# Kernel tuning notes

Hardware: AMD Instinct MI355X
Metric: run time of the kernel (lower is better)

Reference implementation:

```python
import jax, jax.numpy as jnp
import numpy as np

THRESHOLD = 6.0  # bnb MatmulLtState outlier threshold


def setup_inputs() -> dict:
    key = jax.random.key(0)
    k1, k2, k3, k4, k5 = jax.random.split(key, 5)
    B, S, DIN, DOUT = 4, 2048, 4096, 16384
    x = jax.random.normal(k1, (B, S, DIN), dtype=jnp.float32).astype(jnp.float16)
    # inject a few outlier feature columns (|x| > threshold) so the LLM.int8()
    # mixed-precision decomposition path is actually exercised
    out_cols = jax.random.randint(k5, (8,), 0, DIN)
    x = x.at[:, :, out_cols].multiply(10.0)
    # CB: int8 codebook values stored as fp16 (bnb keeps them as int8; math is identical)
    CB = jnp.round(jax.random.uniform(k2, (DOUT, DIN), minval=-127.0, maxval=127.0)).astype(jnp.float16)
    SCB = jax.random.uniform(k3, (DOUT, 1), minval=0.5, maxval=2.0).astype(jnp.float16)
    bias = (jax.random.normal(k4, (DOUT,)) * 0.01).astype(jnp.float16)
    return {"x": x, "CB": CB, "SCB": SCB, "bias": bias}


def _llm_int8_matmul(x, CB, SCB, bias, threshold):
    # forward: weight = CB * SCB / 127 (dequantized fp16 weight), then bnb's
    # mixed int8 matmul with outlier-column decomposition (has_fp16_weights=True)
    W = CB.astype(jnp.float32) * SCB.astype(jnp.float32) / 127.0  # [DOUT, DIN]
    xf = x.astype(jnp.float32)
    lead = xf.shape[:-1]
    X = xf.reshape(-1, xf.shape[-1])  # [N, DIN]

    # outlier columns: any row has |x| > threshold in that feature column
    col_out = (jnp.abs(X) > threshold).any(axis=0)  # [DIN] bool
    X_out = jnp.where(col_out[None, :], X, 0.0)      # fp16-path activations
    X_in = jnp.where(col_out[None, :], 0.0, X)       # int8-path activations

    # per-row (per-token) absmax int8 quantization of inlier activations
    sx = jnp.maximum(jnp.max(jnp.abs(X_in), axis=1, keepdims=True), 1e-8)  # [N,1]
    Xq = jnp.clip(jnp.round(X_in * (127.0 / sx)), -127.0, 127.0)

    # per-output-row absmax int8 quantization of the (dequantized) weight
    sw = jnp.maximum(jnp.max(jnp.abs(W), axis=1, keepdims=True), 1e-8)  # [DOUT,1]
    Wq = jnp.clip(jnp.round(W * (127.0 / sw)), -127.0, 127.0)

    # int8 GEMM (emulated in fp32) + dequant with outer product of scales
    out = (Xq @ Wq.T) * (sx * sw.T) * (1.0 / (127.0 * 127.0))  # [N, DOUT]
    # fp16 outlier path: only the outlier weight columns participate
    out = out + X_out @ jnp.where(col_out[None, :], W, 0.0).T
    out = out + bias.astype(jnp.float32)[None, :]
    return out.reshape(*lead, W.shape[0]).astype(jnp.float16)


def reference(x, CB, SCB, bias):
    return _llm_int8_matmul(x, CB, SCB, bias, THRESHOLD)
```

## Files before the change

### kernel.cpp

```cpp
#include <hip/hip_runtime.h>
#include <hip/hip_fp16.h>
#include <stdint.h>

typedef int v4i __attribute__((ext_vector_type(4)));

__device__ __forceinline__ void gld_lds16(const void* g, void* l) {
    __builtin_amdgcn_global_load_lds(
        (const __attribute__((address_space(1))) void*)g,
        (__attribute__((address_space(3))) void*)l,
        16, 0, 0);
}

#define ENDBAR() do { __builtin_amdgcn_s_barrier(); __builtin_amdgcn_sched_barrier(0); } while (0)
#define VMC(n)   asm volatile("s_waitcnt vmcnt(" #n ")" ::: "memory")
#define VMLG0()  asm volatile("s_waitcnt vmcnt(0) lgkmcnt(0)" ::: "memory")

__global__ __launch_bounds__(256) void k_flags(const float* __restrict__ x,
                                               unsigned int* __restrict__ flags,
                                               int total4, int DIN) {
    int idx = blockIdx.x * blockDim.x + threadIdx.x;
    int stride = gridDim.x * blockDim.x;
    int dmask = DIN - 1;
    for (int i = idx; i < total4; i += stride) {
        float4 v = ((const float4*)x)[i];
        int base = i * 4;
        if (fabsf(v.x) > 6.0f) atomicOr(&flags[(base + 0) & dmask], 1u);
        if (fabsf(v.y) > 6.0f) atomicOr(&flags[(base + 1) & dmask], 1u);
        if (fabsf(v.z) > 6.0f) atomicOr(&flags[(base + 2) & dmask], 1u);
        if (fabsf(v.w) > 6.0f) atomicOr(&flags[(base + 3) & dmask], 1u);
    }
}

__global__ __launch_bounds__(256) void k_build(const unsigned int* __restrict__ flags,
                                               unsigned char* __restrict__ bmask,
                                               int* __restrict__ ncols,
                                               int* __restrict__ cols, int DIN) {
    __shared__ int wcnt[4];
    __shared__ int base;
    int tid = threadIdx.x, lane = tid & 63, wid = tid >> 6;
    if (tid == 0) base = 0;
    __syncthreads();
    for (int c0 = 0; c0 < DIN; c0 += 256) {
        int c = c0 + tid;
        bool p = (c < DIN) && (flags[c] != 0u);
        if (c < DIN) bmask[c] = p ? 1 : 0;
        unsigned long long m = __ballot(p);
        int wpre = __popcll(m & ((1ull << lane) - 1ull));
        if (lane == 0) wcnt[wid] = __popcll(m);
        __syncthreads();
        int pre = 0;
        for (int w = 0; w < wid; w++) pre += wcnt[w];
        if (p) cols[base + pre + wpre] = c;
        __syncthreads();
        if (tid == 0) base += wcnt[0] + wcnt[1] + wcnt[2] + wcnt[3];
        __syncthreads();
    }
    if (tid == 0) *ncols = base;
}

__global__ __launch_bounds__(256) void k_quantx(const float* __restrict__ x,
                                                const unsigned char* __restrict__ bmask,
                                                signed char* __restrict__ Xq,
                                                float* __restrict__ sx,
                                                float* __restrict__ Xout,
                                                const int* __restrict__ ncols,
                                                const int* __restrict__ cols, int DIN) {
    int row = blockIdx.x;
    int tid = threadIdx.x, lane = tid & 63, wid = tid >> 6;
    const float* xr = x + (size_t)row * DIN;
    float f[16];
    #pragma unroll
    for (int j = 0; j < 4; j++) {
        float4 v = ((const float4*)xr)[tid * 4 + j];
        f[4*j] = v.x; f[4*j+1] = v.y; f[4*j+2] = v.z; f[4*j+3] = v.w;
    }
    uint4 bm4 = ((const uint4*)bmask)[tid];
    const unsigned char* bm = (const unsigned char*)&bm4;
    float m = 0.0f;
    #pragma unroll
    for (int j = 0; j < 16; j++) {
        if (bm[j]) f[j] = 0.0f;
        m = fmaxf(m, fabsf(f[j]));
    }
    #pragma unroll
    for (int off = 32; off >= 1; off >>= 1) m = fmaxf(m, __shfl_xor(m, off));
    __shared__ float red[4];
    if (lane == 0) red[wid] = m;
    __syncthreads();
    m = fmaxf(fmaxf(red[0], red[1]), fmaxf(red[2], red[3]));
    float sxv = fmaxf(m, 1e-8f);
    if (Xq) {
        float scale = 127.0f / sxv;
        int qi[16];
        #pragma unroll
        for (int j = 0; j < 16; j++) {
            float r = rintf(f[j] * scale);
            r = fminf(127.0f, fmaxf(-127.0f, r));
            qi[j] = (int)r;
        }
        int4 ov;
        ov.x = (qi[0]&0xff) | ((qi[1]&0xff)<<8) | ((qi[2]&0xff)<<16) | ((qi[3]&0xff)<<24);
        ov.y = (qi[4]&0xff) | ((qi[5]&0xff)<<8) | ((qi[6]&0xff)<<16) | ((qi[7]&0xff)<<24);
        ov.z = (qi[8]&0xff) | ((qi[9]&0xff)<<8) | ((qi[10]&0xff)<<16) | ((qi[11]&0xff)<<24);
        ov.w = (qi[12]&0xff) | ((qi[13]&0xff)<<8) | ((qi[14]&0xff)<<16) | ((qi[15]&0xff)<<24);
        ((int4*)(Xq + (size_t)row * DIN))[tid] = ov;
    }
    if (tid < 16) {
        int nc = *ncols;
        int ncl = nc < 16 ? nc : 16;
        float v = 0.0f;
        if (tid < ncl) v = xr[cols[tid]];
        Xout[(size_t)row * 16 + tid] = v;
    }
    if (tid == 0) sx[row] = sxv;
}

__global__ __launch_bounds__(256) void k_quantw(const float* __restrict__ CB,
                                                const float* __restrict__ SCB,
                                                signed char* __restrict__ Wq,
                                                float* __restrict__ sw,
                                                float* __restrict__ Wout,
                                                const int* __restrict__ ncols,
                                                const int* __restrict__ cols, int DIN) {
    int row = blockIdx.x;
    int tid = threadIdx.x, lane = tid & 63, wid = tid >> 6;
    float scb = SCB[row];
    const float* cr = CB + (size_t)row * DIN;
    float w[16];
    #pragma unroll
    for (int j = 0; j < 4; j++) {
        float4 v = ((const float4*)cr)[tid * 4 + j];
        w[4*j]   = v.x * scb / 127.0f;
        w[4*j+1] = v.y * scb / 127.0f;
        w[4*j+2] = v.z * scb / 127.0f;
        w[4*j+3] = v.w * scb / 127.0f;
    }
    float m = 0.0f;
    #pragma unroll
    for (int j = 0; j < 16; j++) m = fmaxf(m, fabsf(w[j]));
    #pragma unroll
    for (int off = 32; off >= 1; off >>= 1) m = fmaxf(m, __shfl_xor(m, off));
    __shared__ float red[4];
    if (lane == 0) red[wid] = m;
    __syncthreads();
    m = fmaxf(fmaxf(red[0], red[1]), fmaxf(red[2], red[3]));
    float swv = fmaxf(m, 1e-8f);
    if (Wq) {
        float scale = 127.0f / swv;
        int qi[16];
        #pragma unroll
        for (int j = 0; j < 16; j++) {
            float r = rintf(w[j] * scale);
            r = fminf(127.0f, fmaxf(-127.0f, r));
            qi[j] = (int)r;
        }
        int4 ov;
        ov.x = (qi[0]&0xff) | ((qi[1]&0xff)<<8) | ((qi[2]&0xff)<<16) | ((qi[3]&0xff)<<24);
        ov.y = (qi[4]&0xff) | ((qi[5]&0xff)<<8) | ((qi[6]&0xff)<<16) | ((qi[7]&0xff)<<24);
        ov.z = (qi[8]&0xff) | ((qi[9]&0xff)<<8) | ((qi[10]&0xff)<<16) | ((qi[11]&0xff)<<24);
        ov.w = (qi[12]&0xff) | ((qi[13]&0xff)<<8) | ((qi[14]&0xff)<<16) | ((qi[15]&0xff)<<24);
        ((int4*)(Wq + (size_t)row * DIN))[tid] = ov;
    }
    if (tid < 16) {
        int nc = *ncols;
        int ncl = nc < 16 ? nc : 16;
        float v = 0.0f;
        if (tid < ncl) v = cr[cols[tid]] * scb / 127.0f;
        Wout[(size_t)row * 16 + tid] = v;
    }
    if (tid == 0) sw[row] = swv;
}

__global__ __launch_bounds__(512) void k_gemm8(
    const signed char* __restrict__ Xq, const signed char* __restrict__ Wq,
    const float* __restrict__ sx, const float* __restrict__ sw,
    const float* __restrict__ x, const float* __restrict__ CB,
    const float* __restrict__ SCB, const float* __restrict__ bias,
    const float* __restrict__ Xout, const float* __restrict__ Wout,
    const int* __restrict__ ncols, const int* __restrict__ cols,
    float* __restrict__ out, int Nrows, int DOUT, int DIN)
{
    __shared__ __align__(16) char LDS[131072];

    const int tid = threadIdx.x, lane = tid & 63, wid = tid >> 6;
    const int wm = wid >> 2, wn = wid & 3;

    int nwg = gridDim.x, bid = blockIdx.x;
    int swzb;
    if ((nwg & 7) == 0) { int cpx = nwg >> 3; swzb = (bid & 7) * cpx + (bid >> 3); }
    else swzb = bid;
    int mtiles = Nrows >> 8;
    int ntiles = DOUT >> 8;
    int mt, ntl;
    if ((mtiles & 7) == 0 && (ntiles & 3) == 0 && (nwg & 31) == 0) {
        int group = swzb >> 5, local = swzb & 31;
        int mrects = mtiles >> 3;
        int mt_r = group % mrects, nt_r = group / mrects;
        mt  = (mt_r << 3) + (local & 7);
        ntl = (nt_r << 2) + (local >> 3);
    } else {
        mt = swzb % mtiles; ntl = swzb / mtiles;
    }
    int brow = mt << 8, bcol = ntl << 8;

    const int o0 = 16 * ((lane >> 4) ^ ((lane >> 1) & 7));
    const int o1 = o0 ^ 64;
    const int aRow = (wm * 128 + (lane & 15)) * 128;
    const int bRow = (wn * 64 + (lane & 15)) * 128;

    const int stRow = wid * 8 + (lane >> 3);
    const int stCol = 16 * ((lane & 7) ^ (((wid & 1) << 2) + (lane >> 4)));
    const signed char* aSrc = Xq + (size_t)(brow + stRow) * DIN + stCol;
    const signed char* bSrc = Wq + (size_t)(bcol + stRow) * DIN + stCol;
    const int ldsW = wid * 1024;

    v4i acc[8][4] = {};
    v4i a0[8], a1[8], b0[4], b1[4];

    const int nt = DIN >> 7;
    const int NIT = nt >> 1;

#define STAGE_HALF(srcBase, matOff, bf, h, kc)                                   \
    do { _Pragma("unroll")                                                        \
      for (int q = 0; q < 2; q++) {                                               \
        int seg = 2*(h) + q;                                                      \
        gld_lds16((srcBase) + (size_t)seg * 64 * DIN + (kc),                      \
                  &LDS[(matOff) + (bf)*32768 + seg*8192 + ldsW]);                 \
      }                                                                           \
    } while (0)

#define DS_A(dst, bf, miB)                                                        \
    do { _Pragma("unroll")                                                        \
      for (int mi = 0; mi < 4; mi++) {                                            \
        int ro = (bf)*32768 + aRow + ((miB) + mi) * 2048;                         \
        dst[mi*2+0] = *(const v4i*)&LDS[ro + o0];                                 \
        dst[mi*2+1] = *(const v4i*)&LDS[ro + o1];                                 \
      }                                                                           \
    } while (0)

#define DS_B(dst, bf, niB)                                                        \
    do { _Pragma("unroll")                                                        \
      for (int ni = 0; ni < 2; ni++) {                                            \
        int ro = 65536 + (bf)*32768 + bRow + ((niB) + ni) * 2048;                 \
        dst[ni*2+0] = *(const v4i*)&LDS[ro + o0];                                 \
        dst[ni*2+1] = *(const v4i*)&LDS[ro + o1];                                 \
      }                                                                           \
    } while (0)

#define QUAD(A8, B4, accM, accN)                                                  \
    do { __builtin_amdgcn_s_setprio(1); _Pragma("unroll")                         \
      for (int mi = 0; mi < 4; mi++) { _Pragma("unroll")                          \
        for (int ni = 0; ni < 2; ni++) { _Pragma("unroll")                        \
          for (int ks = 0; ks < 2; ks++)                                          \
            acc[(accM)+mi][(accN)+ni] = __builtin_amdgcn_mfma_i32_16x16x64_i8(    \
                A8[mi*2+ks], B4[ni*2+ks], acc[(accM)+mi][(accN)+ni], 0, 0, 0);    \
        } }                                                                       \
      __builtin_amdgcn_s_setprio(0);                                              \
    } while (0)

    STAGE_HALF(aSrc, 0,     0, 0, 0);
    STAGE_HALF(aSrc, 0,     0, 1, 0);
    STAGE_HALF(bSrc, 65536, 0, 0, 0);
    STAGE_HALF(bSrc, 65536, 0, 1, 0);
    STAGE_HALF(aSrc, 0,     1, 0, 128);
    STAGE_HALF(aSrc, 0,     1, 1, 128);
    VMC(4);
    ENDBAR();

    for (int it = 0; it < NIT; ++it) {
        int t = 2 * it;
        int kB1 = (t + 1) << 7;
        int tA2 = t + 2; if (tA2 > nt - 1) tA2 = nt - 1;
        int kA2 = tA2 << 7;
        int tA3 = t + 3; if (tA3 > nt - 1) tA3 = nt - 1;
        int kA3 = tA3 << 7;

        STAGE_HALF(bSrc, 65536, 1, 0, kB1);
        DS_B(b0, 0, 0); DS_A(a0, 0, 0);
        QUAD(a0, b0, 0, 0);
        STAGE_HALF(bSrc, 65536, 1, 1, kB1);
        DS_A(a1, 0, 4);
        QUAD(a1, b0, 4, 0);
        ENDBAR();
        STAGE_HALF(aSrc, 0, 0, 0, kA2);
        DS_B(b1, 0, 2);
        QUAD(a1, b1, 4, 2);
        STAGE_HALF(aSrc, 0, 0, 1, kA2);
        QUAD(a0, b1, 0, 2);
        VMC(4);
        ENDBAR();
        STAGE_HALF(bSrc, 65536, 0, 0, kA2);
        DS_B(b0, 1, 0); DS_A(a0, 1, 0);
        QUAD(a0, b0, 0, 0);
        STAGE_HALF(bSrc, 65536, 0, 1, kA2);
        DS_A(a1, 1, 4);
        QUAD(a1, b0, 4, 0);
        ENDBAR();
        STAGE_HALF(aSrc, 0, 1, 0, kA3);
        DS_B(b1, 1, 2);
        QUAD(a1, b1, 4, 2);
        STAGE_HALF(aSrc, 0, 1, 1, kA3);
        QUAD(a0, b1, 0, 2);
        VMC(4);
        ENDBAR();
    }
    VMLG0();
    ENDBAR();

    int nc = *ncols;
    int ncl = nc < 16 ? nc : 16;
    float* Xo = (float*)&LDS[0];
    float* Wo = (float*)&LDS[65536];
    for (int idx = tid; idx < 4096; idx += 512) {
        int i = idx >> 4, c = idx & 15;
        Xo[i * 17 + c] = Xout[(size_t)(brow + i) * 16 + c];
        Wo[i * 17 + c] = Wout[(size_t)(bcol + i) * 16 + c];
    }
    __syncthreads();

    float sww[4], bzz[4];
    #pragma unroll
    for (int ni = 0; ni < 4; ni++) {
        int gcol = bcol + wn * 64 + ni * 16 + (lane & 15);
        sww[ni] = sw[gcol];
        bzz[ni] = bias[gcol];
    }

    #pragma unroll
    for (int h = 0; h < 2; h++) {
        float vout[4][4][4];
        #pragma unroll
        for (int mi = 0; mi < 4; mi++) {
            int row = wm * 128 + (h * 4 + mi) * 16 + (lane >> 4) * 4;
            #pragma unroll
            for (int r = 0; r < 4; r++) {
                float sxv = sx[brow + row + r];
                #pragma unroll
                for (int ni = 0; ni < 4; ni++)
                    vout[mi][ni][r] =
                        ((float)acc[h * 4 + mi][ni][r] * (sxv * sww[ni])) * (1.0f / 16129.0f);
            }
        }
        for (int c = 0; c < ncl; c++) {
            float wo[4];
            #pragma unroll
            for (int ni = 0; ni < 4; ni++)
                wo[ni] = Wo[(wn * 64 + ni * 16 + (lane & 15)) * 17 + c];
            #pragma unroll
            for (int mi = 0; mi < 4; mi++) {
                int row = wm * 128 + (h * 4 + mi) * 16 + (lane >> 4) * 4;
                #pragma unroll
                for (int r = 0; r < 4; r++) {
                    float xo = Xo[(row + r) * 17 + c];
                    #pragma unroll
                    for (int ni = 0; ni < 4; ni++)
                        vout[mi][ni][r] += xo * wo[ni];
                }
            }
        }
        #pragma unroll
        for (int mi = 0; mi < 4; mi++) {
            #pragma unroll
            for (int ni = 0; ni < 4; ni++) {
                int gcol = bcol + wn * 64 + ni * 16 + (lane & 15);
                #pragma unroll
                for (int r = 0; r < 4; r++) {
                    int grow = brow + wm * 128 + (h * 4 + mi) * 16 + (lane >> 4) * 4 + r;
                    float v = vout[mi][ni][r];
                    for (int c = 16; c < nc; c++) {
                        int col = cols[c];
                        v += x[(size_t)grow * DIN + col] *
                             (CB[(size_t)gcol * DIN + col] * SCB[gcol] / 127.0f);
                    }
                    v += bzz[ni];
                    v = __half2float(__float2half(v));
                    out[(size_t)grow * DOUT + gcol] = v;
                }
            }
        }
    }
#undef STAGE_HALF
#undef DS_A
#undef DS_B
#undef QUAD
}

template<int FLY>
__global__ __launch_bounds__(256) void k_gemm(
    const signed char* __restrict__ Xq, const signed char* __restrict__ Wq,
    const float* __restrict__ sx, const float* __restrict__ sw,
    const float* __restrict__ x, const float* __restrict__ CB,
    const float* __restrict__ SCB, const float* __restrict__ bias,
    const unsigned char* __restrict__ bmask,
    const int* __restrict__ ncols, const int* __restrict__ cols,
    float* __restrict__ out, int Nrows, int DOUT, int DIN)
{
    __shared__ __align__(16) signed char Asm[128 * 64];
    __shared__ __align__(16) signed char Bsm[128 * 64];

    int nwg = gridDim.x;
    int bid = blockIdx.x;
    int swzb;
    if ((nwg & 7) == 0) { int cpx = nwg >> 3; swzb = (bid & 7) * cpx + (bid >> 3); }
    else swzb = bid;
    int mtiles = Nrows >> 7;
    int mt = swzb % mtiles;
    int nt = swzb / mtiles;
    int brow = mt << 7, bcol = nt << 7;

    int tid = threadIdx.x, lane = tid & 63, wid = tid >> 6;
    int wr = wid >> 1, wc = wid & 1;

    v4i acc[4][4] = {};

    int arow = wr * 64 + (lane & 15);
    int brl  = wc * 64 + (lane & 15);
    int kc   = (lane >> 4) * 16;

    if constexpr (FLY == 0) {
        int srow = lane >> 2;
        int scol = (lane & 3) * 16;
        const signed char* ga0 = Xq + (size_t)(brow + wid * 16 + srow) * DIN + scol;
        const signed char* ga1 = Xq + (size_t)(brow + (wid + 4) * 16 + srow) * DIN + scol;
        const signed char* gb0 = Wq + (size_t)(bcol + wid * 16 + srow) * DIN + scol;
        const signed char* gb1 = Wq + (size_t)(bcol + (wid + 4) * 16 + srow) * DIN + scol;
        signed char* la0 = &Asm[wid * 1024];
        signed char* la1 = &Asm[(wid + 4) * 1024];
        signed char* lb0 = &Bsm[wid * 1024];
        signed char* lb1 = &Bsm[(wid + 4) * 1024];

        for (int k0 = 0; k0 < DIN; k0 += 64) {
            gld_lds16(ga0 + k0, la0);
            gld_lds16(ga1 + k0, la1);
            gld_lds16(gb0 + k0, lb0);
            gld_lds16(gb1 + k0, lb1);
            __syncthreads();
            v4i a[4], b[4];
            #pragma unroll
            for (int mi = 0; mi < 4; mi++) a[mi] = *(const v4i*)&Asm[(arow + mi * 16) * 64 + kc];
            #pragma unroll
            for (int ni = 0; ni < 4; ni++) b[ni] = *(const v4i*)&Bsm[(brl + ni * 16) * 64 + kc];
            #pragma unroll
            for (int mi = 0; mi < 4; mi++)
                #pragma unroll
                for (int ni = 0; ni < 4; ni++)
                    acc[mi][ni] = __builtin_amdgcn_mfma_i32_16x16x64_i8(a[mi], b[ni], acc[mi][ni], 0, 0, 0);
            __syncthreads();
        }
    } else {
        int ra = tid >> 1, ca = (tid & 1) * 32;
        const float* xrow = x  + (size_t)(brow + ra) * DIN + ca;
        const float* crow = CB + (size_t)(bcol + ra) * DIN + ca;
        float xscale = 127.0f / sx[brow + ra];
        float scb    = SCB[bcol + ra];
        float wscale = 127.0f / sw[bcol + ra];
        signed char* lda = &Asm[ra * 64 + ca];
        signed char* ldb = &Bsm[ra * 64 + ca];

        for (int k0 = 0; k0 < DIN; k0 += 64) {
            float xa[32], wb[32];
            #pragma unroll
            for (int j = 0; j < 8; j++) {
                float4 v = ((const float4*)(xrow + k0))[j];
                xa[4*j] = v.x; xa[4*j+1] = v.y; xa[4*j+2] = v.z; xa[4*j+3] = v.w;
                float4 u = ((const float4*)(crow + k0))[j];
                wb[4*j] = u.x; wb[4*j+1] = u.y; wb[4*j+2] = u.z; wb[4*j+3] = u.w;
            }
            uint4 bm0 = *(const uint4*)(bmask + k0 + ca);
            uint4 bm1 = *(const uint4*)(bmask + k0 + ca + 16);
            const unsigned char* bmp0 = (const unsigned char*)&bm0;
            const unsigned char* bmp1 = (const unsigned char*)&bm1;
            int qa[32], qb[32];
            #pragma unroll
            for (int j = 0; j < 32; j++) {
                float fx = xa[j];
                if ((j < 16 ? bmp0[j] : bmp1[j - 16])) fx = 0.0f;
                float rx = rintf(fx * xscale);
                qa[j] = (int)fminf(127.0f, fmaxf(-127.0f, rx));
                float wv = wb[j] * scb / 127.0f;
                float rw = rintf(wv * wscale);
                qb[j] = (int)fminf(127.0f, fmaxf(-127.0f, rw));
            }
            int4 pa0, pa1, pb0, pb1;
            #pragma unroll
            for (int g = 0; g < 8; g++) {
                int vpk = (qa[4*g]&0xff) | ((qa[4*g+1]&0xff)<<8) | ((qa[4*g+2]&0xff)<<16) | ((qa[4*g+3]&0xff)<<24);
                if (g < 4) ((int*)&pa0)[g] = vpk; else ((int*)&pa1)[g-4] = vpk;
                int wpk = (qb[4*g]&0xff) | ((qb[4*g+1]&0xff)<<8) | ((qb[4*g+2]&0xff)<<16) | ((qb[4*g+3]&0xff)<<24);
                if (g < 4) ((int*)&pb0)[g] = wpk; else ((int*)&pb1)[g-4] = wpk;
            }
            __syncthreads();
            *(int4*)lda = pa0; *(int4*)(lda + 16) = pa1;
            *(int4*)ldb = pb0; *(int4*)(ldb + 16) = pb1;
            __syncthreads();
            v4i a[4], b[4];
            #pragma unroll
            for (int mi = 0; mi < 4; mi++) a[mi] = *(const v4i*)&Asm[(arow + mi * 16) * 64 + kc];
            #pragma unroll
            for (int ni = 0; ni < 4; ni++) b[ni] = *(const v4i*)&Bsm[(brl + ni * 16) * 64 + kc];
            #pragma unroll
            for (int mi = 0; mi < 4; mi++)
                #pragma unroll
                for (int ni = 0; ni < 4; ni++)
                    acc[mi][ni] = __builtin_amdgcn_mfma_i32_16x16x64_i8(a[mi], b[ni], acc[mi][ni], 0, 0, 0);
        }
        __syncthreads();
    }

    int nc = *ncols;
    int ncl = nc < 16 ? nc : 16;
    float* Xo = (float*)Asm;
    float* Wo = (float*)Bsm;
    for (int idx = tid; idx < 2048; idx += 256) {
        int i = idx >> 4, c = idx & 15;
        if (c < ncl) {
            int col = cols[c];
            Xo[idx] = x[(size_t)(brow + i) * DIN + col];
            Wo[idx] = CB[(size_t)(bcol + i) * DIN + col] * SCB[bcol + i] / 127.0f;
        }
    }
    __syncthreads();

    #pragma unroll
    for (int mi = 0; mi < 4; mi++) {
        #pragma unroll
        for (int ni = 0; ni < 4; ni++) {
            int rl0 = wr * 64 + mi * 16 + (lane >> 4) * 4;
            int cl  = wc * 64 + ni * 16 + (lane & 15);
            int gcol = bcol + cl;
            float swv = sw[gcol];
            float bz = bias[gcol];
            #pragma unroll
            for (int r = 0; r < 4; r++) {
                int grow = brow + rl0 + r;
                float v = ((float)acc[mi][ni][r] * (sx[grow] * swv)) * (1.0f / 16129.0f);
                float osum = 0.0f;
                for (int c = 0; c < ncl; c++)
                    osum += Xo[(rl0 + r) * 16 + c] * Wo[cl * 16 + c];
                for (int c = 16; c < nc; c++) {
                    int col = cols[c];
                    osum += x[(size_t)grow * DIN + col] *
                            (CB[(size_t)gcol * DIN + col] * SCB[gcol] / 127.0f);
                }
                v = v + osum;
                v = v + bz;
                v = __half2float(__float2half(v));
                out[(size_t)grow * DOUT + gcol] = v;
            }
        }
    }
}

static constexpr size_t FLAGS_OFF = 0;
static constexpr size_t BMASK_OFF = 16384;
static constexpr size_t NCOLS_OFF = 20480;
static constexpr size_t COLS_OFF  = 20544;
static constexpr size_t SX_OFF    = 36992;
static constexpr size_t SW_OFF    = 69760;
static constexpr size_t DYN_OFF   = 262144;

extern "C" void kernel_launch(void* const* d_in, const int* in_sizes, int n_in,
                              void* d_out, int out_size, void* d_ws, size_t ws_size,
                              hipStream_t stream) {
    const float* x    = (const float*)d_in[0];
    const float* CB   = (const float*)d_in[1];
    const float* SCB  = (const float*)d_in[2];
    const float* bias = (const float*)d_in[3];

    int DOUT  = in_sizes[2];
    int DIN   = in_sizes[1] / DOUT;
    int Nrows = in_sizes[0] / DIN;

    char* ws = (char*)d_ws;
    unsigned int* flags = (unsigned int*)(ws + FLAGS_OFF);
    unsigned char* bmask = (unsigned char*)(ws + BMASK_OFF);
    int* ncols = (int*)(ws + NCOLS_OFF);
    int* cols  = (int*)(ws + COLS_OFF);
    float* sx  = (float*)(ws + SX_OFF);
    float* sw  = (float*)(ws + SW_OFF);

    size_t off = DYN_OFF;
    float* Xout = (float*)(ws + off); off += (size_t)Nrows * 16 * 4;
    float* Wout = (float*)(ws + off); off += (size_t)DOUT * 16 * 4;
    signed char* Xq = (signed char*)(ws + off); off += (size_t)Nrows * DIN;
    signed char* Wq = (signed char*)(ws + off); off += (size_t)DOUT * DIN;
    size_t need = off;
    float* out = (float*)d_out;

    bool bigws = ws_size >= need;
    bool can8  = bigws && (Nrows % 256 == 0) && (DOUT % 256 == 0) && (DIN % 256 == 0);

    hipMemsetAsync(ws + FLAGS_OFF, 0, 16384, stream);
    k_flags<<<2048, 256, 0, stream>>>(x, flags, Nrows * DIN / 4, DIN);
    k_build<<<1, 256, 0, stream>>>(flags, bmask, ncols, cols, DIN);
    k_quantx<<<Nrows, 256, 0, stream>>>(x, bmask, bigws ? Xq : nullptr, sx,
                                        Xout, ncols, cols, DIN);
    k_quantw<<<DOUT, 256, 0, stream>>>(CB, SCB, bigws ? Wq : nullptr, sw,
                                       Wout, ncols, cols, DIN);

    if (can8) {
        int ngrid = (Nrows / 256) * (DOUT / 256);
        k_gemm8<<<ngrid, 512, 0, stream>>>(Xq, Wq, sx, sw, x, CB, SCB, bias,
                                           Xout, Wout, ncols, cols, out, Nrows, DOUT, DIN);
    } else if (bigws && (Nrows % 128 == 0) && (DOUT % 128 == 0) && (DIN % 64 == 0)) {
        int ngrid = (Nrows / 128) * (DOUT / 128);
        k_gemm<0><<<ngrid, 256, 0, stream>>>(Xq, Wq, sx, sw, x, CB, SCB, bias,
                                             bmask, ncols, cols, out, Nrows, DOUT, DIN);
    } else {
        int ngrid = (Nrows / 128) * (DOUT / 128);
        k_gemm<1><<<ngrid, 256, 0, stream>>>(nullptr, nullptr, sx, sw, x, CB, SCB, bias,
                                             bmask, ncols, cols, out, Nrows, DOUT, DIN);
    }
}
```

Measured before the change: 689.0 us.

## Load A operand directly from global into registers, keep only B in LDS

The int8 GEMM stops staging the activation tile through LDS. Each wave now loads its A fragments straight from global memory into registers (16 v4i per k-step), and only the weight tile is double-buffered in LDS, which halves LDS usage to 64KB. This removes the LDS writes and reads for A and may allow more occupancy. In exchange it adds register pressure, makes the global A loads less coalesced (16-byte per-lane strided rows), and exposes global latency more directly, since A is loaded only one k-step ahead.

```diff
diff --git a/kernel.cpp b/kernel.cpp
--- a/kernel.cpp
+++ b/kernel.cpp
@@ -171,7 +171,7 @@
     if (tid == 0) sw[row] = swv;
 }
 
-__global__ __launch_bounds__(512) void k_gemm8(
+__global__ __launch_bounds__(512) void k_gemmA(
     const signed char* __restrict__ Xq, const signed char* __restrict__ Wq,
     const float* __restrict__ sx, const float* __restrict__ sw,
     const float* __restrict__ x, const float* __restrict__ CB,
@@ -180,7 +180,7 @@
     const int* __restrict__ ncols, const int* __restrict__ cols,
     float* __restrict__ out, int Nrows, int DOUT, int DIN)
 {
-    __shared__ __align__(16) char LDS[131072];
+    __shared__ __align__(16) char LDS[65536];
 
     const int tid = threadIdx.x, lane = tid & 63, wid = tid >> 6;
     const int wm = wid >> 2, wn = wid & 3;
@@ -205,103 +205,99 @@
 
     const int o0 = 16 * ((lane >> 4) ^ ((lane >> 1) & 7));
     const int o1 = o0 ^ 64;
-    const int aRow = (wm * 128 + (lane & 15)) * 128;
     const int bRow = (wn * 64 + (lane & 15)) * 128;
 
     const int stRow = wid * 8 + (lane >> 3);
     const int stCol = 16 * ((lane & 7) ^ (((wid & 1) << 2) + (lane >> 4)));
-    const signed char* aSrc = Xq + (size_t)(brow + stRow) * DIN + stCol;
     const signed char* bSrc = Wq + (size_t)(bcol + stRow) * DIN + stCol;
     const int ldsW = wid * 1024;
 
+    const signed char* aLane =
+        Xq + (size_t)(brow + wm * 128 + (lane & 15)) * DIN + (lane >> 4) * 16;
+
     v4i acc[8][4] = {};
-    v4i a0[8], a1[8], b0[4], b1[4];
+    v4i aA[16];
+    v4i b0[4], b1[4];
 
     const int nt = DIN >> 7;
     const int NIT = nt >> 1;
 
-#define STAGE_HALF(srcBase, matOff, bf, h, kc)                                   \
+#define STAGE_B(bf, h, kc)                                                       \
     do { _Pragma("unroll")                                                        \
       for (int q = 0; q < 2; q++) {                                               \
         int seg = 2*(h) + q;                                                      \
-        gld_lds16((srcBase) + (size_t)seg * 64 * DIN + (kc),                      \
-                  &LDS[(matOff) + (bf)*32768 + seg*8192 + ldsW]);                 \
+        gld_lds16(bSrc + (size_t)seg * 64 * DIN + (kc),                           \
+                  &LDS[(bf)*32768 + seg*8192 + ldsW]);                            \
       }                                                                           \
     } while (0)
 
-#define DS_A(dst, bf, miB)                                                        \
+#define LOAD_A(kc)                                                                \
     do { _Pragma("unroll")                                                        \
-      for (int mi = 0; mi < 4; mi++) {                                            \
-        int ro = (bf)*32768 + aRow + ((miB) + mi) * 2048;                         \
-        dst[mi*2+0] = *(const v4i*)&LDS[ro + o0];                                 \
-        dst[mi*2+1] = *(const v4i*)&LDS[ro + o1];                                 \
+      for (int mi = 0; mi < 8; mi++) { _Pragma("unroll")                          \
+        for (int ks = 0; ks < 2; ks++)                                            \
+          aA[mi*2+ks] = *(const v4i*)(aLane + (size_t)mi * 16 * DIN +             \
+                                      (kc) + ks * 64);                            \
       }                                                                           \
     } while (0)
 
 #define DS_B(dst, bf, niB)                                                        \
     do { _Pragma("unroll")                                                        \
       for (int ni = 0; ni < 2; ni++) {                                            \
-        int ro = 65536 + (bf)*32768 + bRow + ((niB) + ni) * 2048;                 \
+        int ro = (bf)*32768 + bRow + ((niB) + ni) * 2048;                         \
         dst[ni*2+0] = *(const v4i*)&LDS[ro + o0];                                 \
         dst[ni*2+1] = *(const v4i*)&LDS[ro + o1];                                 \
       }                                                                           \
     } while (0)
 
-#define QUAD(A8, B4, accM, accN)                                                  \
+#define QUADH(miB, B4, accN)                                                      \
     do { __builtin_amdgcn_s_setprio(1); _Pragma("unroll")                         \
       for (int mi = 0; mi < 4; mi++) { _Pragma("unroll")                          \
         for (int ni = 0; ni < 2; ni++) { _Pragma("unroll")                        \
           for (int ks = 0; ks < 2; ks++)                                          \
-            acc[(accM)+mi][(accN)+ni] = __builtin_amdgcn_mfma_i32_16x16x64_i8(    \
-                A8[mi*2+ks], B4[ni*2+ks], acc[(accM)+mi][(accN)+ni], 0, 0, 0);    \
+            acc[(miB)+mi][(accN)+ni] = __builtin_amdgcn_mfma_i32_16x16x64_i8(     \
+                aA[((miB)+mi)*2+ks], B4[ni*2+ks],                                 \
+                acc[(miB)+mi][(accN)+ni], 0, 0, 0);                               \
         } }                                                                       \
       __builtin_amdgcn_s_setprio(0);                                              \
     } while (0)
 
-    STAGE_HALF(aSrc, 0,     0, 0, 0);
-    STAGE_HALF(aSrc, 0,     0, 1, 0);
-    STAGE_HALF(bSrc, 65536, 0, 0, 0);
-    STAGE_HALF(bSrc, 65536, 0, 1, 0);
-    STAGE_HALF(aSrc, 0,     1, 0, 128);
-    STAGE_HALF(aSrc, 0,     1, 1, 128);
-    VMC(4);
+    LOAD_A(0);
+    STAGE_B(0, 0, 0);
+    STAGE_B(0, 1, 0);
+    VMC(0);
     ENDBAR();
 
     for (int it = 0; it < NIT; ++it) {
         int t = 2 * it;
         int kB1 = (t + 1) << 7;
-        int tA2 = t + 2; if (tA2 > nt - 1) tA2 = nt - 1;
-        int kA2 = tA2 << 7;
-        int tA3 = t + 3; if (tA3 > nt - 1) tA3 = nt - 1;
-        int kA3 = tA3 << 7;
-
-        STAGE_HALF(bSrc, 65536, 1, 0, kB1);
-        DS_B(b0, 0, 0); DS_A(a0, 0, 0);
-        QUAD(a0, b0, 0, 0);
-        STAGE_HALF(bSrc, 65536, 1, 1, kB1);
-        DS_A(a1, 0, 4);
-        QUAD(a1, b0, 4, 0);
+        int tA1 = t + 1; if (tA1 > nt - 1) tA1 = nt - 1;
+        int kA1 = tA1 << 7;
+        int tN2 = t + 2; if (tN2 > nt - 1) tN2 = nt - 1;
+        int kN2 = tN2 << 7;
+
+        STAGE_B(1, 0, kB1);
+        DS_B(b0, 0, 0);
+        QUADH(0, b0, 0);
+        STAGE_B(1, 1, kB1);
+        QUADH(4, b0, 0);
         ENDBAR();
-        STAGE_HALF(aSrc, 0, 0, 0, kA2);
         DS_B(b1, 0, 2);
-        QUAD(a1, b1, 4, 2);
-        STAGE_HALF(aSrc, 0, 0, 1, kA2);
-        QUAD(a0, b1, 0, 2);
-        VMC(4);
+        QUADH(4, b1, 2);
+        QUADH(0, b1, 2);
+        LOAD_A(kA1);
+        VMC(16);
         ENDBAR();
-        STAGE_HALF(bSrc, 65536, 0, 0, kA2);
-        DS_B(b0, 1, 0); DS_A(a0, 1, 0);
-        QUAD(a0, b0, 0, 0);
-        STAGE_HALF(bSrc, 65536, 0, 1, kA2);
-        DS_A(a1, 1, 4);
-        QUAD(a1, b0, 4, 0);
+        STAGE_B(0, 0, kN2);
+        DS_B(b0, 1, 0);
+        QUADH(0, b0, 0);
+        STAGE_B(0, 1, kN2);
+        QUADH(4, b0, 0);
         ENDBAR();
-        STAGE_HALF(aSrc, 0, 1, 0, kA3);
         DS_B(b1, 1, 2);
-        QUAD(a1, b1, 4, 2);
-        STAGE_HALF(aSrc, 0, 1, 1, kA3);
-        QUAD(a0, b1, 0, 2);
-        VMC(4);
+        QUADH(4, b1, 2);
+        QUADH(0, b1, 2);
+        LOAD_A(kN2);
+        VMC(16);
         ENDBAR();
     }
     VMLG0();
@@ -310,7 +306,7 @@
     int nc = *ncols;
     int ncl = nc < 16 ? nc : 16;
     float* Xo = (float*)&LDS[0];
-    float* Wo = (float*)&LDS[65536];
+    float* Wo = (float*)&LDS[32768];
     for (int idx = tid; idx < 4096; idx += 512) {
         int i = idx >> 4, c = idx & 15;
         Xo[i * 17 + c] = Xout[(size_t)(brow + i) * 16 + c];
@@ -379,10 +375,10 @@
             }
         }
     }
-#undef STAGE_HALF
-#undef DS_A
+#undef STAGE_B
+#undef LOAD_A
 #undef DS_B
-#undef QUAD
+#undef QUADH
 }
 
 template<int FLY>
@@ -600,7 +596,7 @@
 
     if (can8) {
         int ngrid = (Nrows / 256) * (DOUT / 256);
-        k_gemm8<<<ngrid, 512, 0, stream>>>(Xq, Wq, sx, sw, x, CB, SCB, bias,
+        k_gemmA<<<ngrid, 512, 0, stream>>>(Xq, Wq, sx, sw, x, CB, SCB, bias,
                                            Xout, Wout, ncols, cols, out, Nrows, DOUT, DIN);
     } else if (bigws && (Nrows % 128 == 0) && (DOUT % 128 == 0) && (DIN % 64 == 0)) {
         int ngrid = (Nrows / 128) * (DOUT / 128);
```

Result: slower. 1.523 ms (+121.0%).
